# Kernel optimization log

Hardware: AMD Instinct MI355X
Metric: run time of the kernel (lower is better)

## Reference

```python
import jax, jax.numpy as jnp
import numpy as np

W, HN, C, NHEAD = 256, 128, 512, 8


def layer_norm(x, w, b, eps=1e-5):
    m = x.mean(-1, keepdims=True)
    v = ((x - m) ** 2).mean(-1, keepdims=True)
    return (x - m) / jnp.sqrt(v + eps) * w + b


def setup_inputs() -> dict:
    key = jax.random.key(0)
    ks = jax.random.split(key, 6)
    s = 0.02
    return {
        "feat_left": jax.random.normal(ks[0], (W, HN, C), jnp.float32),
        "feat_right": jax.random.normal(ks[1], (W, HN, C), jnp.float32),
        "pos": jax.random.normal(ks[2], (2 * W - 1, C), jnp.float32),
        "pos_indexes": jax.random.randint(ks[3], (W * W,), 0, 2 * W - 1, dtype=jnp.int32),
        "ln_w": jnp.ones((C,), jnp.float32),
        "ln_b": jnp.zeros((C,), jnp.float32),
        "in_proj_w": jax.random.normal(ks[4], (3 * C, C), jnp.float32) * s,
        "in_proj_b": jnp.zeros((3 * C,), jnp.float32),
        "out_w": jax.random.normal(ks[5], (C, C), jnp.float32) * s,
        "out_b": jnp.zeros((C,), jnp.float32),
    }


def reference(feat_left, feat_right, pos, pos_indexes, ln_w, ln_b, in_proj_w, in_proj_b, out_w, out_b):
    w, n, c = feat_left.shape
    e = NHEAD
    hd = c // e
    scaling = hd ** -0.5

    # pre-norm (same norm1 applied to both streams)
    ql = layer_norm(feat_left, ln_w, ln_b)     # [W,N,C]
    kv_in = layer_norm(feat_right, ln_w, ln_b)  # [W,N,C]

    # cross-attn projections: q from left with in_proj[:C], k/v from right with in_proj[C:]
    q = ql @ in_proj_w[:c].T + in_proj_b[:c]
    kv = kv_in @ in_proj_w[c:].T + in_proj_b[c:]
    k, v = jnp.split(kv, 2, axis=-1)

    # relative pos encoding gather: [2W-1,C] -> [W*W,C] -> [W,W',C]
    pe = pos[pos_indexes].reshape(w, w, c)
    qr_kr = pe @ in_proj_w[: 2 * c].T + in_proj_b[: 2 * c]
    q_r, k_r = jnp.split(qr_kr, 2, axis=-1)

    q = (q * scaling).reshape(w, n, e, hd)
    q_r = (q_r * scaling).reshape(w, w, e, hd)
    k = k.reshape(w, n, e, hd)
    v = v.reshape(w, n, e, hd)
    k_r = k_r.reshape(w, w, e, hd)

    # content-content + content-pos + pos-content scores: [N,E,W,W']
    attn = (jnp.einsum('wnec,vnec->newv', q, k)
            + jnp.einsum('wnec,wvec->newv', q, k_r)
            + jnp.einsum('vnec,wvec->newv', k, q_r))

    raw_attn = attn.sum(axis=1)                      # [N,W,W']
    p = jax.nn.softmax(attn, axis=-1)
    v_o = jnp.einsum('newv,vnec->wnec', p, v).reshape(w, n, c)
    v_o = v_o @ out_w.T + out_b

    return feat_left + v_o, raw_attn
```

## Files before the change

### kernel.cpp

```cpp
#include <hip/hip_runtime.h>

#define WW 256
#define NB 128
#define CD 512
#define NE 8
#define HD 64
#define NCHUNKS 4
#define SCALING 0.125f

typedef __attribute__((ext_vector_type(8))) short bfx8;
typedef __attribute__((ext_vector_type(4))) float fx4;

#define OFF_MEAN   0u
#define OFF_RSTD   65536u
#define OFF_WPB    131072u
#define OFF_OWB    524288u
#define OFF_S      655360u
#define OFF_U      656896u
#define OFF_PQ     658432u
#define OFF_PK     789504u
#define OFF_QB     920576u
#define OFF_KB     9309184u
#define OFF_VB     17697792u
#define OFF_ATTN   26086400u
#define OFF_T3     42863616u
#define OFF_PB     51252224u
#define OFF_VOB    59640832u

__device__ __forceinline__ unsigned short f2bf(float f) {
  unsigned u = __builtin_bit_cast(unsigned, f);
  u = (u + 0x7fffu + ((u >> 16) & 1u)) >> 16;
  return (unsigned short)u;
}
__device__ __forceinline__ float bf2f(unsigned short h) {
  unsigned u = ((unsigned)h) << 16;
  return __builtin_bit_cast(float, u);
}

#define GLDS16(g, l)                                                          \
  __builtin_amdgcn_global_load_lds(                                           \
      (const __attribute__((address_space(1))) void*)(g),                     \
      (__attribute__((address_space(3))) void*)(l), 16, 0, 0)

__global__ __launch_bounds__(256) void cvt_kernel(const float* __restrict__ a,
                                                  unsigned short* __restrict__ b,
                                                  int n8) {
  int i = blockIdx.x * 256 + threadIdx.x;
  if (i >= n8) return;
  float4 x = ((const float4*)a)[2 * i];
  float4 y = ((const float4*)a)[2 * i + 1];
  int4 o;
  o.x = (int)(((unsigned)f2bf(x.y) << 16) | f2bf(x.x));
  o.y = (int)(((unsigned)f2bf(x.w) << 16) | f2bf(x.z));
  o.z = (int)(((unsigned)f2bf(y.y) << 16) | f2bf(y.x));
  o.w = (int)(((unsigned)f2bf(y.w) << 16) | f2bf(y.z));
  ((int4*)b)[i] = o;
}

__global__ __launch_bounds__(256) void stats_kernel(const float* __restrict__ L,
                                                    const float* __restrict__ R,
                                                    float* __restrict__ mean,
                                                    float* __restrict__ rstd,
                                                    unsigned short* __restrict__ flb,
                                                    unsigned short* __restrict__ frb) {
  int wave = threadIdx.x >> 6, lane = threadIdx.x & 63;
  int row = blockIdx.x * 4 + wave;
  const float* src = (row < 32768) ? (L + (size_t)row * CD) : (R + (size_t)(row - 32768) * CD);
  unsigned short* drow = (row < 32768) ? (flb + (size_t)row * CD) : (frb + (size_t)(row - 32768) * CD);
  float4 a = *(const float4*)(src + lane * 4);
  float4 b = *(const float4*)(src + 256 + lane * 4);
  short4 sa, sb;
  sa.x = (short)f2bf(a.x); sa.y = (short)f2bf(a.y); sa.z = (short)f2bf(a.z); sa.w = (short)f2bf(a.w);
  sb.x = (short)f2bf(b.x); sb.y = (short)f2bf(b.y); sb.z = (short)f2bf(b.z); sb.w = (short)f2bf(b.w);
  *(short4*)(drow + lane * 4) = sa;
  *(short4*)(drow + 256 + lane * 4) = sb;
  float s  = a.x + a.y + a.z + a.w + b.x + b.y + b.z + b.w;
  float ss = a.x*a.x + a.y*a.y + a.z*a.z + a.w*a.w + b.x*b.x + b.y*b.y + b.z*b.z + b.w*b.w;
#pragma unroll
  for (int off = 32; off > 0; off >>= 1) {
    s  += __shfl_xor(s, off);
    ss += __shfl_xor(ss, off);
  }
  if (lane == 0) {
    float m = s * (1.0f / 512.0f);
    float v = ss * (1.0f / 512.0f) - m * m;
    mean[row] = m;
    rstd[row] = rsqrtf(v + 1e-5f);
  }
}

__global__ __launch_bounds__(256) void prep_kernel(const float* __restrict__ ipw,
                                                   const float* __restrict__ ipb,
                                                   const float* __restrict__ lnw,
                                                   const float* __restrict__ lnb,
                                                   unsigned short* __restrict__ Wpb,
                                                   float* __restrict__ S,
                                                   float* __restrict__ U) {
  int o = blockIdx.x, t = threadIdx.x;
  float s = 0.f, u = 0.f;
#pragma unroll
  for (int j0 = 0; j0 < 512; j0 += 256) {
    int j = j0 + t;
    float w0 = ipw[(size_t)o * 512 + j];
    float wl = w0 * lnw[j];
    unsigned short h = f2bf(wl);
    Wpb[(size_t)o * 512 + j] = h;
    s += bf2f(h);
    u += w0 * lnb[j];
  }
  __shared__ float rs[4], ru[4];
  int lane = t & 63, wv = t >> 6;
#pragma unroll
  for (int off = 32; off > 0; off >>= 1) { s += __shfl_xor(s, off); u += __shfl_xor(u, off); }
  if (lane == 0) { rs[wv] = s; ru[wv] = u; }
  __syncthreads();
  if (t == 0) {
    S[o] = rs[0] + rs[1] + rs[2] + rs[3];
    U[o] = ru[0] + ru[1] + ru[2] + ru[3] + ipb[o];
  }
}

__global__ __launch_bounds__(256) void gemm_ln(const unsigned short* __restrict__ A,
                                               const unsigned short* __restrict__ Bw,
                                               const float* __restrict__ S,
                                               const float* __restrict__ U,
                                               const float* __restrict__ mean,
                                               const float* __restrict__ rstd,
                                               unsigned short* __restrict__ out0,
                                               unsigned short* __restrict__ out1,
                                               int wOff, int statOff, float scale) {
  __shared__ unsigned short As[128 * 32];
  __shared__ unsigned short Bs[128 * 32];
  int t = threadIdx.x;
  int lane = t & 63, w = t >> 6;
  int quad = lane >> 4, l15 = lane & 15;
  int wm = w >> 1, wn = w & 1;
  int m0 = blockIdx.x * 128, n0 = blockIdx.y * 128;

  unsigned short* ldsA0 = As + (size_t)w * 16 * 32;
  unsigned short* ldsA1 = As + (size_t)(64 + w * 16) * 32;
  unsigned short* ldsB0 = Bs + (size_t)w * 16 * 32;
  unsigned short* ldsB1 = Bs + (size_t)(64 + w * 16) * 32;
  const unsigned short* gA0 = A + (size_t)(m0 + w * 16 + (lane >> 2)) * 512 + (lane & 3) * 8;
  const unsigned short* gA1 = gA0 + (size_t)64 * 512;
  const unsigned short* gB0 = Bw + (size_t)(wOff + n0 + w * 16 + (lane >> 2)) * 512 + (lane & 3) * 8;
  const unsigned short* gB1 = gB0 + (size_t)64 * 512;

  fx4 acc[4][4];
#pragma unroll
  for (int i = 0; i < 4; ++i)
#pragma unroll
    for (int j = 0; j < 4; ++j) acc[i][j] = (fx4){0.f, 0.f, 0.f, 0.f};

  for (int kt = 0; kt < 512; kt += 32) {
    GLDS16(gA0 + kt, ldsA0);
    GLDS16(gA1 + kt, ldsA1);
    GLDS16(gB0 + kt, ldsB0);
    GLDS16(gB1 + kt, ldsB1);
    __syncthreads();
    bfx8 af[4], bfr[4];
#pragma unroll
    for (int i = 0; i < 4; ++i)
      af[i] = *(const bfx8*)(As + (size_t)(wm * 64 + i * 16 + l15) * 32 + quad * 8);
#pragma unroll
    for (int j = 0; j < 4; ++j)
      bfr[j] = *(const bfx8*)(Bs + (size_t)(wn * 64 + j * 16 + l15) * 32 + quad * 8);
#pragma unroll
    for (int i = 0; i < 4; ++i)
#pragma unroll
      for (int j = 0; j < 4; ++j)
        acc[i][j] = __builtin_amdgcn_mfma_f32_16x16x32_bf16(af[i], bfr[j], acc[i][j], 0, 0, 0);
    __syncthreads();
  }

  float mn[16], rs[16];
#pragma unroll
  for (int i = 0; i < 4; ++i)
#pragma unroll
    for (int r = 0; r < 4; ++r) {
      int m = statOff + m0 + wm * 64 + i * 16 + quad * 4 + r;
      mn[i * 4 + r] = mean[m];
      rs[i * 4 + r] = rstd[m];
    }
#pragma unroll
  for (int j = 0; j < 4; ++j) {
    int oc = n0 + wn * 64 + j * 16 + l15;
    int o = wOff + oc;
    float Sv = S[o], Uv = U[o];
    unsigned short* dst; int cc;
    if (oc < 512) { dst = out0; cc = oc; } else { dst = out1; cc = oc - 512; }
#pragma unroll
    for (int i = 0; i < 4; ++i)
#pragma unroll
      for (int r = 0; r < 4; ++r) {
        int m = m0 + wm * 64 + i * 16 + quad * 4 + r;
        dst[(size_t)m * 512 + cc] =
            f2bf(((acc[i][j][r] - mn[i * 4 + r] * Sv) * rs[i * 4 + r] + Uv) * scale);
      }
  }
}

__global__ __launch_bounds__(256) void gemm_out(const unsigned short* __restrict__ A,
                                                const unsigned short* __restrict__ Bw,
                                                const float* __restrict__ ob,
                                                const float* __restrict__ fl,
                                                float* __restrict__ out, int wc) {
  __shared__ unsigned short As[128 * 32];
  __shared__ unsigned short Bs[128 * 32];
  int t = threadIdx.x;
  int lane = t & 63, w = t >> 6;
  int quad = lane >> 4, l15 = lane & 15;
  int wm = w >> 1, wn = w & 1;
  int n0 = blockIdx.x * 128, m0 = blockIdx.y * 128;

  unsigned short* ldsA0 = As + (size_t)w * 16 * 32;
  unsigned short* ldsA1 = As + (size_t)(64 + w * 16) * 32;
  unsigned short* ldsB0 = Bs + (size_t)w * 16 * 32;
  unsigned short* ldsB1 = Bs + (size_t)(64 + w * 16) * 32;
  const unsigned short* gA0 = A + (size_t)(m0 + w * 16 + (lane >> 2)) * 512 + (lane & 3) * 8;
  const unsigned short* gA1 = gA0 + (size_t)64 * 512;
  const unsigned short* gB0 = Bw + (size_t)(n0 + w * 16 + (lane >> 2)) * 512 + (lane & 3) * 8;
  const unsigned short* gB1 = gB0 + (size_t)64 * 512;

  fx4 acc[4][4];
#pragma unroll
  for (int i = 0; i < 4; ++i)
#pragma unroll
    for (int j = 0; j < 4; ++j) acc[i][j] = (fx4){0.f, 0.f, 0.f, 0.f};

  for (int kt = 0; kt < 512; kt += 32) {
    GLDS16(gA0 + kt, ldsA0);
    GLDS16(gA1 + kt, ldsA1);
    GLDS16(gB0 + kt, ldsB0);
    GLDS16(gB1 + kt, ldsB1);
    __syncthreads();
    bfx8 af[4], bfr[4];
#pragma unroll
    for (int i = 0; i < 4; ++i)
      af[i] = *(const bfx8*)(As + (size_t)(wm * 64 + i * 16 + l15) * 32 + quad * 8);
#pragma unroll
    for (int j = 0; j < 4; ++j)
      bfr[j] = *(const bfx8*)(Bs + (size_t)(wn * 64 + j * 16 + l15) * 32 + quad * 8);
#pragma unroll
    for (int i = 0; i < 4; ++i)
#pragma unroll
      for (int j = 0; j < 4; ++j)
        acc[i][j] = __builtin_amdgcn_mfma_f32_16x16x32_bf16(af[i], bfr[j], acc[i][j], 0, 0, 0);
    __syncthreads();
  }

  size_t gbase = (size_t)wc * 64 * NB * CD;
#pragma unroll
  for (int j = 0; j < 4; ++j) {
    int o = n0 + wn * 64 + j * 16 + l15;
    float bias = ob[o];
#pragma unroll
    for (int i = 0; i < 4; ++i)
#pragma unroll
      for (int r = 0; r < 4; ++r) {
        int m = m0 + wm * 64 + i * 16 + quad * 4 + r;
        size_t go = gbase + (size_t)m * 512 + o;
        out[go] = acc[i][j][r] + bias + fl[go];
      }
  }
}

__device__ __forceinline__ void compute16(const float* __restrict__ As,
                                          const float* __restrict__ Bs,
                                          float acc[4][4], int tx, int ty) {
#pragma unroll
  for (int kk = 0; kk < 16; ++kk) {
    float4 av = *(const float4*)(As + kk * 64 + ty * 4);
    float4 bv = *(const float4*)(Bs + kk * 64 + tx * 4);
    const float aa[4] = {av.x, av.y, av.z, av.w};
    const float bb[4] = {bv.x, bv.y, bv.z, bv.w};
#pragma unroll
    for (int i = 0; i < 4; ++i)
#pragma unroll
      for (int j = 0; j < 4; ++j)
        acc[i][j] = fmaf(aa[i], bb[j], acc[i][j]);
  }
}

__global__ __launch_bounds__(256) void posproj_kernel(const float* __restrict__ pos,
                                                      const float* __restrict__ ipw,
                                                      const float* __restrict__ ipb,
                                                      unsigned short* __restrict__ Pq,
                                                      unsigned short* __restrict__ Pk) {
  __shared__ float As[16 * 64], Bs[16 * 64];
  int t = threadIdx.x, tx = t & 15, ty = t >> 4;
  int n0 = blockIdx.x * 64, m0 = blockIdx.y * 64;
  int lr = t >> 2, lq = t & 3;
  int arow = m0 + lr; if (arow > 510) arow = 510;
  const float* xrow = pos + (size_t)arow * 512 + lq * 4;
  const float* wrow = ipw + (size_t)(n0 + lr) * 512 + lq * 4;
  float acc[4][4] = {};
  for (int kt = 0; kt < 512; kt += 16) {
    float4 a = *(const float4*)(xrow + kt);
    float4 b = *(const float4*)(wrow + kt);
    __syncthreads();
    As[(lq * 4 + 0) * 64 + lr] = a.x; As[(lq * 4 + 1) * 64 + lr] = a.y;
    As[(lq * 4 + 2) * 64 + lr] = a.z; As[(lq * 4 + 3) * 64 + lr] = a.w;
    Bs[(lq * 4 + 0) * 64 + lr] = b.x; Bs[(lq * 4 + 1) * 64 + lr] = b.y;
    Bs[(lq * 4 + 2) * 64 + lr] = b.z; Bs[(lq * 4 + 3) * 64 + lr] = b.w;
    __syncthreads();
    compute16(As, Bs, acc, tx, ty);
  }
  float scale = (n0 < 512) ? SCALING : 1.0f;
  unsigned short* dst; int co;
  if (n0 < 512) { dst = Pq; co = n0; } else { dst = Pk; co = n0 - 512; }
#pragma unroll
  for (int i = 0; i < 4; ++i) {
    int m = m0 + ty * 4 + i;
    if (m < 511) {
      short4 r;
      r.x = (short)f2bf((acc[i][0] + ipb[n0 + tx * 4 + 0]) * scale);
      r.y = (short)f2bf((acc[i][1] + ipb[n0 + tx * 4 + 1]) * scale);
      r.z = (short)f2bf((acc[i][2] + ipb[n0 + tx * 4 + 2]) * scale);
      r.w = (short)f2bf((acc[i][3] + ipb[n0 + tx * 4 + 3]) * scale);
      *(short4*)(dst + (size_t)m * 512 + co + tx * 4) = r;
    }
  }
}

__global__ __launch_bounds__(256) void t3_kernel(const unsigned short* __restrict__ kb,
                                                 const unsigned short* __restrict__ Pq,
                                                 const int* __restrict__ idx,
                                                 unsigned short* __restrict__ T3, int wc) {
  __shared__ unsigned short As[128 * 72];
  __shared__ unsigned short Bs[64 * 72];
  int t = threadIdx.x, lane = t & 63, w = t >> 6;
  int quad = lane >> 4, l15 = lane & 15;
  int e = blockIdx.x, v = blockIdx.y;
  const unsigned short* asrc = kb + ((size_t)v * NB) * 512 + e * 64;
  for (int c = t; c < 1024; c += 256) {
    int row = c >> 3, c8 = c & 7;
    *(int4*)(As + row * 72 + c8 * 8) = *(const int4*)(asrc + (size_t)row * 512 + c8 * 8);
  }
  for (int c = t; c < 512; c += 256) {
    int row = c >> 3, c8 = c & 7;
    int ri = idx[(wc * 64 + row) * WW + v];
    *(int4*)(Bs + row * 72 + c8 * 8) = *(const int4*)(Pq + (size_t)ri * 512 + e * 64 + c8 * 8);
  }
  __syncthreads();
  fx4 acc[2][4];
#pragma unroll
  for (int i = 0; i < 2; ++i)
#pragma unroll
    for (int j = 0; j < 4; ++j) acc[i][j] = (fx4){0.f, 0.f, 0.f, 0.f};
#pragma unroll
  for (int kt = 0; kt < 64; kt += 32) {
    bfx8 af[2], bfr[4];
#pragma unroll
    for (int i = 0; i < 2; ++i)
      af[i] = *(const bfx8*)(As + (w * 32 + i * 16 + l15) * 72 + kt + quad * 8);
#pragma unroll
    for (int j = 0; j < 4; ++j)
      bfr[j] = *(const bfx8*)(Bs + (j * 16 + l15) * 72 + kt + quad * 8);
#pragma unroll
    for (int i = 0; i < 2; ++i)
#pragma unroll
      for (int j = 0; j < 4; ++j)
        acc[i][j] = __builtin_amdgcn_mfma_f32_16x16x32_bf16(af[i], bfr[j], acc[i][j], 0, 0, 0);
  }
#pragma unroll
  for (int i = 0; i < 2; ++i)
#pragma unroll
    for (int j = 0; j < 4; ++j)
#pragma unroll
      for (int r = 0; r < 4; ++r) {
        int n = w * 32 + i * 16 + quad * 4 + r;
        int wq = j * 16 + l15;
        T3[(((size_t)e * WW + v) * NB + n) * 64 + wq] = f2bf(acc[i][j][r]);
      }
}

__global__ __launch_bounds__(256) void t1_kernel(const unsigned short* __restrict__ qb,
                                                 const unsigned short* __restrict__ kb,
                                                 const unsigned short* __restrict__ T3,
                                                 float* __restrict__ attn, int wc) {
  __shared__ unsigned short As[64 * 72];
  __shared__ unsigned short Bs[256 * 72];
  int t = threadIdx.x, lane = t & 63, w = t >> 6;
  int quad = lane >> 4, l15 = lane & 15;
  int e = blockIdx.x, n = blockIdx.y;
  const unsigned short* asrc = qb + ((size_t)(wc * 64) * NB + n) * 512 + e * 64;
  for (int c = t; c < 512; c += 256) {
    int row = c >> 3, c8 = c & 7;
    *(int4*)(As + row * 72 + c8 * 8) = *(const int4*)(asrc + (size_t)row * NB * 512 + c8 * 8);
  }
  const unsigned short* bsrc = kb + (size_t)n * 512 + e * 64;
  for (int c = t; c < 2048; c += 256) {
    int row = c >> 3, c8 = c & 7;
    *(int4*)(Bs + row * 72 + c8 * 8) = *(const int4*)(bsrc + (size_t)row * NB * 512 + c8 * 8);
  }
  __syncthreads();
  fx4 acc[4][4];
#pragma unroll
  for (int i = 0; i < 4; ++i)
#pragma unroll
    for (int j = 0; j < 4; ++j) acc[i][j] = (fx4){0.f, 0.f, 0.f, 0.f};
#pragma unroll
  for (int kt = 0; kt < 64; kt += 32) {
    bfx8 af[4], bfr[4];
#pragma unroll
    for (int i = 0; i < 4; ++i)
      af[i] = *(const bfx8*)(As + (i * 16 + l15) * 72 + kt + quad * 8);
#pragma unroll
    for (int j = 0; j < 4; ++j)
      bfr[j] = *(const bfx8*)(Bs + (w * 64 + j * 16 + l15) * 72 + kt + quad * 8);
#pragma unroll
    for (int i = 0; i < 4; ++i)
#pragma unroll
      for (int j = 0; j < 4; ++j)
        acc[i][j] = __builtin_amdgcn_mfma_f32_16x16x32_bf16(af[i], bfr[j], acc[i][j], 0, 0, 0);
  }
  __syncthreads();
  const unsigned short* tsrc = T3 + ((size_t)e * WW * NB + n) * 64;
  for (int c = t; c < 2048; c += 256) {
    int row = c >> 3, c8 = c & 7;
    *(int4*)(Bs + row * 72 + c8 * 8) = *(const int4*)(tsrc + (size_t)row * NB * 64 + c8 * 8);
  }
  __syncthreads();
#pragma unroll
  for (int i = 0; i < 4; ++i)
#pragma unroll
    for (int j = 0; j < 4; ++j) {
      int vg = w * 64 + j * 16 + l15;
      ushort4 t3v = *(const ushort4*)(Bs + (size_t)vg * 72 + i * 16 + quad * 4);
      const unsigned short tv[4] = {t3v.x, t3v.y, t3v.z, t3v.w};
#pragma unroll
      for (int r = 0; r < 4; ++r) {
        int wq = i * 16 + quad * 4 + r;
        float* p = attn + (((size_t)n * NE + e) * 64 + wq) * WW + vg;
        *p = acc[i][j][r] + bf2f(tv[r]);
      }
    }
}

__global__ __launch_bounds__(256) void t2s_kernel(const unsigned short* __restrict__ qb,
                                                  const unsigned short* __restrict__ Pk,
                                                  const int* __restrict__ idx,
                                                  const float* __restrict__ attn,
                                                  unsigned short* __restrict__ pbuf,
                                                  float* __restrict__ raw, int wc) {
  __shared__ unsigned short As[16 * 72];
  __shared__ unsigned short Bs[256 * 72];
  __shared__ int idxs[256];
  __shared__ float redm[16 * 4];
  __shared__ float reds[16 * 4];
  int t = threadIdx.x, lane = t & 63, w = t >> 6;
  int quad = lane >> 4, l15 = lane & 15;
  int wq = blockIdx.x, nt = blockIdx.y;
  int n0 = nt * 16;
  idxs[t] = idx[((size_t)(wc * 64 + wq)) * WW + t];

  fx4 raws[4];
#pragma unroll
  for (int j = 0; j < 4; ++j) raws[j] = (fx4){0.f, 0.f, 0.f, 0.f};

  const unsigned short* abase = qb + ((size_t)(wc * 64 + wq) * NB + n0) * 512;

  for (int e = 0; e < NE; ++e) {
    __syncthreads();
    if (t < 128) {
      int row = t >> 3, c8 = t & 7;
      *(int4*)(As + row * 72 + c8 * 8) = *(const int4*)(abase + (size_t)row * 512 + e * 64 + c8 * 8);
    }
    for (int c = t; c < 2048; c += 256) {
      int row = c >> 3, c8 = c & 7;
      int ri = idxs[row];
      *(int4*)(Bs + row * 72 + c8 * 8) = *(const int4*)(Pk + (size_t)ri * 512 + e * 64 + c8 * 8);
    }
    __syncthreads();

    fx4 acc[4];
#pragma unroll
    for (int j = 0; j < 4; ++j) acc[j] = (fx4){0.f, 0.f, 0.f, 0.f};
    bfx8 af0 = *(const bfx8*)(As + l15 * 72 + quad * 8);
    bfx8 af1 = *(const bfx8*)(As + l15 * 72 + 32 + quad * 8);
#pragma unroll
    for (int j = 0; j < 4; ++j) {
      bfx8 b0 = *(const bfx8*)(Bs + (w * 64 + j * 16 + l15) * 72 + quad * 8);
      acc[j] = __builtin_amdgcn_mfma_f32_16x16x32_bf16(af0, b0, acc[j], 0, 0, 0);
    }
#pragma unroll
    for (int j = 0; j < 4; ++j) {
      bfx8 b1 = *(const bfx8*)(Bs + (w * 64 + j * 16 + l15) * 72 + 32 + quad * 8);
      acc[j] = __builtin_amdgcn_mfma_f32_16x16x32_bf16(af1, b1, acc[j], 0, 0, 0);
    }

#pragma unroll
    for (int j = 0; j < 4; ++j) {
      int vg = w * 64 + j * 16 + l15;
#pragma unroll
      for (int r = 0; r < 4; ++r) {
        int n = n0 + quad * 4 + r;
        acc[j][r] += attn[(((size_t)n * NE + e) * 64 + wq) * WW + vg];
      }
    }

    float rm[4];
#pragma unroll
    for (int r = 0; r < 4; ++r)
      rm[r] = fmaxf(fmaxf(acc[0][r], acc[1][r]), fmaxf(acc[2][r], acc[3][r]));
#pragma unroll
    for (int off = 1; off < 16; off <<= 1)
#pragma unroll
      for (int r = 0; r < 4; ++r) rm[r] = fmaxf(rm[r], __shfl_xor(rm[r], off));
    if (l15 == 0) {
#pragma unroll
      for (int r = 0; r < 4; ++r) redm[(quad * 4 + r) * 4 + w] = rm[r];
    }
    __syncthreads();
    float fm[4];
#pragma unroll
    for (int r = 0; r < 4; ++r) {
      const float* rp = redm + (quad * 4 + r) * 4;
      fm[r] = fmaxf(fmaxf(rp[0], rp[1]), fmaxf(rp[2], rp[3]));
    }
    float ex[4][4];
    float ls[4] = {0.f, 0.f, 0.f, 0.f};
#pragma unroll
    for (int j = 0; j < 4; ++j)
#pragma unroll
      for (int r = 0; r < 4; ++r) {
        ex[j][r] = __expf(acc[j][r] - fm[r]);
        ls[r] += ex[j][r];
      }
#pragma unroll
    for (int off = 1; off < 16; off <<= 1)
#pragma unroll
      for (int r = 0; r < 4; ++r) ls[r] += __shfl_xor(ls[r], off);
    if (l15 == 0) {
#pragma unroll
      for (int r = 0; r < 4; ++r) reds[(quad * 4 + r) * 4 + w] = ls[r];
    }
    __syncthreads();
    float inv[4];
#pragma unroll
    for (int r = 0; r < 4; ++r) {
      const float* sp = reds + (quad * 4 + r) * 4;
      inv[r] = 1.0f / (sp[0] + sp[1] + sp[2] + sp[3]);
    }
#pragma unroll
    for (int j = 0; j < 4; ++j) {
      int vg = w * 64 + j * 16 + l15;
#pragma unroll
      for (int r = 0; r < 4; ++r) {
        int n = n0 + quad * 4 + r;
        pbuf[(((size_t)n * NE + e) * 64 + wq) * WW + vg] = f2bf(ex[j][r] * inv[r]);
        raws[j][r] += acc[j][r];
      }
    }
  }

#pragma unroll
  for (int j = 0; j < 4; ++j) {
    int vg = w * 64 + j * 16 + l15;
#pragma unroll
    for (int r = 0; r < 4; ++r) {
      int n = n0 + quad * 4 + r;
      raw[((size_t)n * WW + wc * 64 + wq) * WW + vg] = raws[j][r];
    }
  }
}

__global__ __launch_bounds__(256) void pv_kernel(const unsigned short* __restrict__ pb,
                                                 const unsigned short* __restrict__ vb,
                                                 unsigned short* __restrict__ vob) {
  __shared__ unsigned short As[64 * 72];
  __shared__ unsigned short Bs[64 * 72];
  int t = threadIdx.x, lane = t & 63, w = t >> 6;
  int quad = lane >> 4, l15 = lane & 15;
  int e = blockIdx.x, n = blockIdx.y;
  fx4 acc[4];
#pragma unroll
  for (int j = 0; j < 4; ++j) acc[j] = (fx4){0.f, 0.f, 0.f, 0.f};
  const unsigned short* abase = pb + (((size_t)n * NE + e) * 64) * WW;
  for (int kc = 0; kc < 4; ++kc) {
    for (int c = t; c < 512; c += 256) {
      int row = c >> 3, c8 = c & 7;
      *(int4*)(As + row * 72 + c8 * 8) = *(const int4*)(abase + (size_t)row * WW + kc * 64 + c8 * 8);
    }
    for (int c = t; c < 512; c += 256) {
      int row = c >> 3, c8 = c & 7;
      *(int4*)(Bs + row * 72 + c8 * 8) =
          *(const int4*)(vb + ((size_t)(kc * 64 + row) * NB + n) * 512 + e * 64 + c8 * 8);
    }
    __syncthreads();
#pragma unroll
    for (int kt = 0; kt < 64; kt += 32) {
      bfx8 af = *(const bfx8*)(As + (w * 16 + l15) * 72 + kt + quad * 8);
      bfx8 bfr[4];
#pragma unroll
      for (int j = 0; j < 4; ++j)
        bfr[j] = *(const bfx8*)(Bs + (j * 16 + l15) * 72 + kt + quad * 8);
#pragma unroll
      for (int j = 0; j < 4; ++j)
        acc[j] = __builtin_amdgcn_mfma_f32_16x16x32_bf16(af, bfr[j], acc[j], 0, 0, 0);
    }
    __syncthreads();
  }
#pragma unroll
  for (int j = 0; j < 4; ++j)
#pragma unroll
    for (int r = 0; r < 4; ++r) {
      int wq = w * 16 + quad * 4 + r;
      vob[((size_t)wq * NB + n) * 512 + e * 64 + j * 16 + l15] = f2bf(acc[j][r]);
    }
}

extern "C" void kernel_launch(void* const* d_in, const int* in_sizes, int n_in,
                              void* d_out, int out_size, void* d_ws, size_t ws_size,
                              hipStream_t stream) {
  const float* fl  = (const float*)d_in[0];
  const float* fr  = (const float*)d_in[1];
  const float* pos = (const float*)d_in[2];
  const int*  pidx = (const int*)d_in[3];
  const float* lnw = (const float*)d_in[4];
  const float* lnb = (const float*)d_in[5];
  const float* ipw = (const float*)d_in[6];
  const float* ipb = (const float*)d_in[7];
  const float* ow  = (const float*)d_in[8];
  const float* ob  = (const float*)d_in[9];

  float* ws   = (float*)d_ws;
  float* mean = ws + OFF_MEAN;
  float* rstd = ws + OFF_RSTD;
  unsigned short* Wpb = (unsigned short*)(ws + OFF_WPB);
  unsigned short* owb = (unsigned short*)(ws + OFF_OWB);
  float* S    = ws + OFF_S;
  float* U    = ws + OFF_U;
  unsigned short* Pq = (unsigned short*)(ws + OFF_PQ);
  unsigned short* Pk = (unsigned short*)(ws + OFF_PK);
  unsigned short* qb = (unsigned short*)(ws + OFF_QB);
  unsigned short* kb = (unsigned short*)(ws + OFF_KB);
  unsigned short* vb = (unsigned short*)(ws + OFF_VB);
  float* attn = ws + OFF_ATTN;
  unsigned short* T3  = (unsigned short*)(ws + OFF_T3);
  unsigned short* pb  = (unsigned short*)(ws + OFF_PB);
  unsigned short* vob = (unsigned short*)(ws + OFF_VOB);
  unsigned short* flb = (unsigned short*)(ws + OFF_ATTN);
  unsigned short* frb = flb + (size_t)32768 * 512;

  float* outF = (float*)d_out;
  float* outR = outF + (size_t)WW * NB * CD;

  stats_kernel<<<16384, 256, 0, stream>>>(fl, fr, mean, rstd, flb, frb);
  prep_kernel<<<1536, 256, 0, stream>>>(ipw, ipb, lnw, lnb, Wpb, S, U);
  cvt_kernel<<<128, 256, 0, stream>>>(ow, owb, 32768);
  posproj_kernel<<<dim3(16, 8), 256, 0, stream>>>(pos, ipw, ipb, Pq, Pk);
  gemm_ln<<<dim3(256, 4), 256, 0, stream>>>(flb, Wpb, S, U, mean, rstd, qb, qb, 0, 0, SCALING);
  gemm_ln<<<dim3(256, 8), 256, 0, stream>>>(frb, Wpb, S, U, mean, rstd, kb, vb, 512, 32768, 1.0f);

  for (int wc = 0; wc < NCHUNKS; ++wc) {
    t3_kernel<<<dim3(8, 256), 256, 0, stream>>>(kb, Pq, pidx, T3, wc);
    t1_kernel<<<dim3(8, 128), 256, 0, stream>>>(qb, kb, T3, attn, wc);
    t2s_kernel<<<dim3(64, 8), 256, 0, stream>>>(qb, Pk, pidx, attn, pb, outR, wc);
    pv_kernel<<<dim3(8, 128), 256, 0, stream>>>(pb, vb, vob);
    gemm_out<<<dim3(4, 64), 256, 0, stream>>>(vob, owb, ob, fl, outF, wc);
  }
}
```

Measured before the change: 841.6 us.

## Double-buffer GEMM LDS tiles with XOR swizzle and move pos projection to MFMA

The gemm_ln and gemm_out kernels now double-buffer their LDS tiles, so the global-to-LDS load of the next K slice is issued before computing the current one. They also XOR-swizzle the LDS column layout to reduce bank conflicts. The fp32 FMA position-projection kernel is replaced by a bf16 MFMA GEMM, which needs extra conversion kernels for pos and in_proj_w. This doubles LDS use per block and adds custom waitcnt and barrier sequencing, which must be exactly right to avoid races.

```diff
diff --git a/kernel.cpp b/kernel.cpp
--- a/kernel.cpp
+++ b/kernel.cpp
@@ -129,21 +129,20 @@
                                                unsigned short* __restrict__ out0,
                                                unsigned short* __restrict__ out1,
                                                int wOff, int statOff, float scale) {
-  __shared__ unsigned short As[128 * 32];
-  __shared__ unsigned short Bs[128 * 32];
+  __shared__ unsigned short As[2][128 * 32];
+  __shared__ unsigned short Bs[2][128 * 32];
   int t = threadIdx.x;
   int lane = t & 63, w = t >> 6;
   int quad = lane >> 4, l15 = lane & 15;
   int wm = w >> 1, wn = w & 1;
   int m0 = blockIdx.x * 128, n0 = blockIdx.y * 128;
 
-  unsigned short* ldsA0 = As + (size_t)w * 16 * 32;
-  unsigned short* ldsA1 = As + (size_t)(64 + w * 16) * 32;
-  unsigned short* ldsB0 = Bs + (size_t)w * 16 * 32;
-  unsigned short* ldsB1 = Bs + (size_t)(64 + w * 16) * 32;
-  const unsigned short* gA0 = A + (size_t)(m0 + w * 16 + (lane >> 2)) * 512 + (lane & 3) * 8;
+  int cs = ((lane & 3) ^ ((lane >> 3) & 3)) * 8;
+  unsigned lo0 = (unsigned)(w * 16) * 32;
+  unsigned lo1 = (unsigned)(64 + w * 16) * 32;
+  const unsigned short* gA0 = A + (size_t)(m0 + w * 16 + (lane >> 2)) * 512 + cs;
   const unsigned short* gA1 = gA0 + (size_t)64 * 512;
-  const unsigned short* gB0 = Bw + (size_t)(wOff + n0 + w * 16 + (lane >> 2)) * 512 + (lane & 3) * 8;
+  const unsigned short* gB0 = Bw + (size_t)(wOff + n0 + w * 16 + (lane >> 2)) * 512 + cs;
   const unsigned short* gB1 = gB0 + (size_t)64 * 512;
 
   fx4 acc[4][4];
@@ -152,26 +151,51 @@
 #pragma unroll
     for (int j = 0; j < 4; ++j) acc[i][j] = (fx4){0.f, 0.f, 0.f, 0.f};
 
-  for (int kt = 0; kt < 512; kt += 32) {
-    GLDS16(gA0 + kt, ldsA0);
-    GLDS16(gA1 + kt, ldsA1);
-    GLDS16(gB0 + kt, ldsB0);
-    GLDS16(gB1 + kt, ldsB1);
-    __syncthreads();
-    bfx8 af[4], bfr[4];
-#pragma unroll
-    for (int i = 0; i < 4; ++i)
-      af[i] = *(const bfx8*)(As + (size_t)(wm * 64 + i * 16 + l15) * 32 + quad * 8);
-#pragma unroll
-    for (int j = 0; j < 4; ++j)
-      bfr[j] = *(const bfx8*)(Bs + (size_t)(wn * 64 + j * 16 + l15) * 32 + quad * 8);
-#pragma unroll
-    for (int i = 0; i < 4; ++i)
-#pragma unroll
-      for (int j = 0; j < 4; ++j)
-        acc[i][j] = __builtin_amdgcn_mfma_f32_16x16x32_bf16(af[i], bfr[j], acc[i][j], 0, 0, 0);
-    __syncthreads();
-  }
+  int ro = (quad ^ ((l15 >> 1) & 3)) * 8;
+
+#define STAGE_G(buf, kk)                                                      \
+  do {                                                                        \
+    GLDS16(gA0 + (kk), &As[buf][lo0]);                                        \
+    GLDS16(gA1 + (kk), &As[buf][lo1]);                                        \
+    GLDS16(gB0 + (kk), &Bs[buf][lo0]);                                        \
+    GLDS16(gB1 + (kk), &Bs[buf][lo1]);                                        \
+  } while (0)
+
+#define COMPUTE_G(buf)                                                        \
+  do {                                                                        \
+    const unsigned short* Ab = &As[buf][0];                                   \
+    const unsigned short* Bb = &Bs[buf][0];                                   \
+    bfx8 af[4], bfr[4];                                                       \
+    _Pragma("unroll")                                                         \
+    for (int i = 0; i < 4; ++i)                                               \
+      af[i] = *(const bfx8*)(Ab + (size_t)(wm * 64 + i * 16 + l15) * 32 + ro);\
+    _Pragma("unroll")                                                         \
+    for (int j = 0; j < 4; ++j)                                               \
+      bfr[j] = *(const bfx8*)(Bb + (size_t)(wn * 64 + j * 16 + l15) * 32 + ro);\
+    _Pragma("unroll")                                                         \
+    for (int i = 0; i < 4; ++i)                                               \
+      _Pragma("unroll")                                                       \
+      for (int j = 0; j < 4; ++j)                                             \
+        acc[i][j] = __builtin_amdgcn_mfma_f32_16x16x32_bf16(af[i], bfr[j], acc[i][j], 0, 0, 0); \
+  } while (0)
+
+  STAGE_G(0, 0);
+  int cur = 0;
+  for (int kt = 0; kt < 480; kt += 32) {
+    STAGE_G(cur ^ 1, kt + 32);
+    asm volatile("s_waitcnt vmcnt(4)" ::: "memory");
+    __builtin_amdgcn_s_barrier();
+    __builtin_amdgcn_sched_barrier(0);
+    COMPUTE_G(cur);
+    asm volatile("s_waitcnt lgkmcnt(0)" ::: "memory");
+    __builtin_amdgcn_s_barrier();
+    __builtin_amdgcn_sched_barrier(0);
+    cur ^= 1;
+  }
+  asm volatile("s_waitcnt vmcnt(0)" ::: "memory");
+  __builtin_amdgcn_s_barrier();
+  __builtin_amdgcn_sched_barrier(0);
+  COMPUTE_G(cur);
 
   float mn[16], rs[16];
 #pragma unroll
@@ -198,6 +222,8 @@
             f2bf(((acc[i][j][r] - mn[i * 4 + r] * Sv) * rs[i * 4 + r] + Uv) * scale);
       }
   }
+#undef STAGE_G
+#undef COMPUTE_G
 }
 
 __global__ __launch_bounds__(256) void gemm_out(const unsigned short* __restrict__ A,
@@ -205,21 +231,20 @@
                                                 const float* __restrict__ ob,
                                                 const float* __restrict__ fl,
                                                 float* __restrict__ out, int wc) {
-  __shared__ unsigned short As[128 * 32];
-  __shared__ unsigned short Bs[128 * 32];
+  __shared__ unsigned short As[2][128 * 32];
+  __shared__ unsigned short Bs[2][128 * 32];
   int t = threadIdx.x;
   int lane = t & 63, w = t >> 6;
   int quad = lane >> 4, l15 = lane & 15;
   int wm = w >> 1, wn = w & 1;
   int n0 = blockIdx.x * 128, m0 = blockIdx.y * 128;
 
-  unsigned short* ldsA0 = As + (size_t)w * 16 * 32;
-  unsigned short* ldsA1 = As + (size_t)(64 + w * 16) * 32;
-  unsigned short* ldsB0 = Bs + (size_t)w * 16 * 32;
-  unsigned short* ldsB1 = Bs + (size_t)(64 + w * 16) * 32;
-  const unsigned short* gA0 = A + (size_t)(m0 + w * 16 + (lane >> 2)) * 512 + (lane & 3) * 8;
+  int cs = ((lane & 3) ^ ((lane >> 3) & 3)) * 8;
+  unsigned lo0 = (unsigned)(w * 16) * 32;
+  unsigned lo1 = (unsigned)(64 + w * 16) * 32;
+  const unsigned short* gA0 = A + (size_t)(m0 + w * 16 + (lane >> 2)) * 512 + cs;
   const unsigned short* gA1 = gA0 + (size_t)64 * 512;
-  const unsigned short* gB0 = Bw + (size_t)(n0 + w * 16 + (lane >> 2)) * 512 + (lane & 3) * 8;
+  const unsigned short* gB0 = Bw + (size_t)(n0 + w * 16 + (lane >> 2)) * 512 + cs;
   const unsigned short* gB1 = gB0 + (size_t)64 * 512;
 
   fx4 acc[4][4];
@@ -228,26 +253,51 @@
 #pragma unroll
     for (int j = 0; j < 4; ++j) acc[i][j] = (fx4){0.f, 0.f, 0.f, 0.f};
 
-  for (int kt = 0; kt < 512; kt += 32) {
-    GLDS16(gA0 + kt, ldsA0);
-    GLDS16(gA1 + kt, ldsA1);
-    GLDS16(gB0 + kt, ldsB0);
-    GLDS16(gB1 + kt, ldsB1);
-    __syncthreads();
-    bfx8 af[4], bfr[4];
-#pragma unroll
-    for (int i = 0; i < 4; ++i)
-      af[i] = *(const bfx8*)(As + (size_t)(wm * 64 + i * 16 + l15) * 32 + quad * 8);
-#pragma unroll
-    for (int j = 0; j < 4; ++j)
-      bfr[j] = *(const bfx8*)(Bs + (size_t)(wn * 64 + j * 16 + l15) * 32 + quad * 8);
-#pragma unroll
-    for (int i = 0; i < 4; ++i)
-#pragma unroll
-      for (int j = 0; j < 4; ++j)
-        acc[i][j] = __builtin_amdgcn_mfma_f32_16x16x32_bf16(af[i], bfr[j], acc[i][j], 0, 0, 0);
-    __syncthreads();
-  }
+  int ro = (quad ^ ((l15 >> 1) & 3)) * 8;
+
+#define STAGE_O(buf, kk)                                                      \
+  do {                                                                        \
+    GLDS16(gA0 + (kk), &As[buf][lo0]);                                        \
+    GLDS16(gA1 + (kk), &As[buf][lo1]);                                        \
+    GLDS16(gB0 + (kk), &Bs[buf][lo0]);                                        \
+    GLDS16(gB1 + (kk), &Bs[buf][lo1]);                                        \
+  } while (0)
+
+#define COMPUTE_O(buf)                                                        \
+  do {                                                                        \
+    const unsigned short* Ab = &As[buf][0];                                   \
+    const unsigned short* Bb = &Bs[buf][0];                                   \
+    bfx8 af[4], bfr[4];                                                       \
+    _Pragma("unroll")                                                         \
+    for (int i = 0; i < 4; ++i)                                               \
+      af[i] = *(const bfx8*)(Ab + (size_t)(wm * 64 + i * 16 + l15) * 32 + ro);\
+    _Pragma("unroll")                                                         \
+    for (int j = 0; j < 4; ++j)                                               \
+      bfr[j] = *(const bfx8*)(Bb + (size_t)(wn * 64 + j * 16 + l15) * 32 + ro);\
+    _Pragma("unroll")                                                         \
+    for (int i = 0; i < 4; ++i)                                               \
+      _Pragma("unroll")                                                       \
+      for (int j = 0; j < 4; ++j)                                             \
+        acc[i][j] = __builtin_amdgcn_mfma_f32_16x16x32_bf16(af[i], bfr[j], acc[i][j], 0, 0, 0); \
+  } while (0)
+
+  STAGE_O(0, 0);
+  int cur = 0;
+  for (int kt = 0; kt < 480; kt += 32) {
+    STAGE_O(cur ^ 1, kt + 32);
+    asm volatile("s_waitcnt vmcnt(4)" ::: "memory");
+    __builtin_amdgcn_s_barrier();
+    __builtin_amdgcn_sched_barrier(0);
+    COMPUTE_O(cur);
+    asm volatile("s_waitcnt lgkmcnt(0)" ::: "memory");
+    __builtin_amdgcn_s_barrier();
+    __builtin_amdgcn_sched_barrier(0);
+    cur ^= 1;
+  }
+  asm volatile("s_waitcnt vmcnt(0)" ::: "memory");
+  __builtin_amdgcn_s_barrier();
+  __builtin_amdgcn_sched_barrier(0);
+  COMPUTE_O(cur);
 
   size_t gbase = (size_t)wc * 64 * NB * CD;
 #pragma unroll
@@ -263,64 +313,103 @@
         out[go] = acc[i][j][r] + bias + fl[go];
       }
   }
-}
-
-__device__ __forceinline__ void compute16(const float* __restrict__ As,
-                                          const float* __restrict__ Bs,
-                                          float acc[4][4], int tx, int ty) {
-#pragma unroll
-  for (int kk = 0; kk < 16; ++kk) {
-    float4 av = *(const float4*)(As + kk * 64 + ty * 4);
-    float4 bv = *(const float4*)(Bs + kk * 64 + tx * 4);
-    const float aa[4] = {av.x, av.y, av.z, av.w};
-    const float bb[4] = {bv.x, bv.y, bv.z, bv.w};
+#undef STAGE_O
+#undef COMPUTE_O
+}
+
+__global__ __launch_bounds__(256) void posproj_mfma(const unsigned short* __restrict__ Apos,
+                                                    const unsigned short* __restrict__ Bw,
+                                                    const float* __restrict__ ipb,
+                                                    unsigned short* __restrict__ Pq,
+                                                    unsigned short* __restrict__ Pk) {
+  __shared__ unsigned short As[2][128 * 32];
+  __shared__ unsigned short Bs[2][128 * 32];
+  int t = threadIdx.x;
+  int lane = t & 63, w = t >> 6;
+  int quad = lane >> 4, l15 = lane & 15;
+  int wm = w >> 1, wn = w & 1;
+  int m0 = blockIdx.x * 128, n0 = blockIdx.y * 128;
+
+  int cs = ((lane & 3) ^ ((lane >> 3) & 3)) * 8;
+  unsigned lo0 = (unsigned)(w * 16) * 32;
+  unsigned lo1 = (unsigned)(64 + w * 16) * 32;
+  int ar0 = m0 + w * 16 + (lane >> 2); if (ar0 > 510) ar0 = 510;
+  int ar1 = m0 + 64 + w * 16 + (lane >> 2); if (ar1 > 510) ar1 = 510;
+  const unsigned short* gA0 = Apos + (size_t)ar0 * 512 + cs;
+  const unsigned short* gA1 = Apos + (size_t)ar1 * 512 + cs;
+  const unsigned short* gB0 = Bw + (size_t)(n0 + w * 16 + (lane >> 2)) * 512 + cs;
+  const unsigned short* gB1 = gB0 + (size_t)64 * 512;
+
+  fx4 acc[4][4];
+#pragma unroll
+  for (int i = 0; i < 4; ++i)
+#pragma unroll
+    for (int j = 0; j < 4; ++j) acc[i][j] = (fx4){0.f, 0.f, 0.f, 0.f};
+
+  int ro = (quad ^ ((l15 >> 1) & 3)) * 8;
+
+#define STAGE_P(buf, kk)                                                      \
+  do {                                                                        \
+    GLDS16(gA0 + (kk), &As[buf][lo0]);                                        \
+    GLDS16(gA1 + (kk), &As[buf][lo1]);                                        \
+    GLDS16(gB0 + (kk), &Bs[buf][lo0]);                                        \
+    GLDS16(gB1 + (kk), &Bs[buf][lo1]);                                        \
+  } while (0)
+
+#define COMPUTE_P(buf)                                                        \
+  do {                                                                        \
+    const unsigned short* Ab = &As[buf][0];                                   \
+    const unsigned short* Bb = &Bs[buf][0];                                   \
+    bfx8 af[4], bfr[4];                                                       \
+    _Pragma("unroll")                                                         \
+    for (int i = 0; i < 4; ++i)                                               \
+      af[i] = *(const bfx8*)(Ab + (size_t)(wm * 64 + i * 16 + l15) * 32 + ro);\
+    _Pragma("unroll")                                                         \
+    for (int j = 0; j < 4; ++j)                                               \
+      bfr[j] = *(const bfx8*)(Bb + (size_t)(wn * 64 + j * 16 + l15) * 32 + ro);\
+    _Pragma("unroll")                                                         \
+    for (int i = 0; i < 4; ++i)                                               \
+      _Pragma("unroll")                                                       \
+      for (int j = 0; j < 4; ++j)                                             \
+        acc[i][j] = __builtin_amdgcn_mfma_f32_16x16x32_bf16(af[i], bfr[j], acc[i][j], 0, 0, 0); \
+  } while (0)
+
+  STAGE_P(0, 0);
+  int cur = 0;
+  for (int kt = 0; kt < 480; kt += 32) {
+    STAGE_P(cur ^ 1, kt + 32);
+    asm volatile("s_waitcnt vmcnt(4)" ::: "memory");
+    __builtin_amdgcn_s_barrier();
+    __builtin_amdgcn_sched_barrier(0);
+    COMPUTE_P(cur);
+    asm volatile("s_waitcnt lgkmcnt(0)" ::: "memory");
+    __builtin_amdgcn_s_barrier();
+    __builtin_amdgcn_sched_barrier(0);
+    cur ^= 1;
+  }
+  asm volatile("s_waitcnt vmcnt(0)" ::: "memory");
+  __builtin_amdgcn_s_barrier();
+  __builtin_amdgcn_sched_barrier(0);
+  COMPUTE_P(cur);
+
+#pragma unroll
+  for (int j = 0; j < 4; ++j) {
+    int o = n0 + wn * 64 + j * 16 + l15;
+    float bias = ipb[o];
+    float scale = (o < 512) ? SCALING : 1.0f;
+    unsigned short* dst; int cc;
+    if (o < 512) { dst = Pq; cc = o; } else { dst = Pk; cc = o - 512; }
 #pragma unroll
     for (int i = 0; i < 4; ++i)
 #pragma unroll
-      for (int j = 0; j < 4; ++j)
-        acc[i][j] = fmaf(aa[i], bb[j], acc[i][j]);
-  }
-}
-
-__global__ __launch_bounds__(256) void posproj_kernel(const float* __restrict__ pos,
-                                                      const float* __restrict__ ipw,
-                                                      const float* __restrict__ ipb,
-                                                      unsigned short* __restrict__ Pq,
-                                                      unsigned short* __restrict__ Pk) {
-  __shared__ float As[16 * 64], Bs[16 * 64];
-  int t = threadIdx.x, tx = t & 15, ty = t >> 4;
-  int n0 = blockIdx.x * 64, m0 = blockIdx.y * 64;
-  int lr = t >> 2, lq = t & 3;
-  int arow = m0 + lr; if (arow > 510) arow = 510;
-  const float* xrow = pos + (size_t)arow * 512 + lq * 4;
-  const float* wrow = ipw + (size_t)(n0 + lr) * 512 + lq * 4;
-  float acc[4][4] = {};
-  for (int kt = 0; kt < 512; kt += 16) {
-    float4 a = *(const float4*)(xrow + kt);
-    float4 b = *(const float4*)(wrow + kt);
-    __syncthreads();
-    As[(lq * 4 + 0) * 64 + lr] = a.x; As[(lq * 4 + 1) * 64 + lr] = a.y;
-    As[(lq * 4 + 2) * 64 + lr] = a.z; As[(lq * 4 + 3) * 64 + lr] = a.w;
-    Bs[(lq * 4 + 0) * 64 + lr] = b.x; Bs[(lq * 4 + 1) * 64 + lr] = b.y;
-    Bs[(lq * 4 + 2) * 64 + lr] = b.z; Bs[(lq * 4 + 3) * 64 + lr] = b.w;
-    __syncthreads();
-    compute16(As, Bs, acc, tx, ty);
-  }
-  float scale = (n0 < 512) ? SCALING : 1.0f;
-  unsigned short* dst; int co;
-  if (n0 < 512) { dst = Pq; co = n0; } else { dst = Pk; co = n0 - 512; }
-#pragma unroll
-  for (int i = 0; i < 4; ++i) {
-    int m = m0 + ty * 4 + i;
-    if (m < 511) {
-      short4 r;
-      r.x = (short)f2bf((acc[i][0] + ipb[n0 + tx * 4 + 0]) * scale);
-      r.y = (short)f2bf((acc[i][1] + ipb[n0 + tx * 4 + 1]) * scale);
-      r.z = (short)f2bf((acc[i][2] + ipb[n0 + tx * 4 + 2]) * scale);
-      r.w = (short)f2bf((acc[i][3] + ipb[n0 + tx * 4 + 3]) * scale);
-      *(short4*)(dst + (size_t)m * 512 + co + tx * 4) = r;
-    }
-  }
+      for (int r = 0; r < 4; ++r) {
+        int m = m0 + wm * 64 + i * 16 + quad * 4 + r;
+        if (m < 511)
+          dst[(size_t)m * 512 + cc] = f2bf((acc[i][j][r] + bias) * scale);
+      }
+  }
+#undef STAGE_P
+#undef COMPUTE_P
 }
 
 __global__ __launch_bounds__(256) void t3_kernel(const unsigned short* __restrict__ kb,
@@ -643,6 +732,8 @@
   unsigned short* vob = (unsigned short*)(ws + OFF_VOB);
   unsigned short* flb = (unsigned short*)(ws + OFF_ATTN);
   unsigned short* frb = flb + (size_t)32768 * 512;
+  unsigned short* posb = (unsigned short*)(ws + OFF_T3);
+  unsigned short* ipwb = posb + 262144;
 
   float* outF = (float*)d_out;
   float* outR = outF + (size_t)WW * NB * CD;
@@ -650,7 +741,9 @@
   stats_kernel<<<16384, 256, 0, stream>>>(fl, fr, mean, rstd, flb, frb);
   prep_kernel<<<1536, 256, 0, stream>>>(ipw, ipb, lnw, lnb, Wpb, S, U);
   cvt_kernel<<<128, 256, 0, stream>>>(ow, owb, 32768);
-  posproj_kernel<<<dim3(16, 8), 256, 0, stream>>>(pos, ipw, ipb, Pq, Pk);
+  cvt_kernel<<<128, 256, 0, stream>>>(pos, posb, 32704);
+  cvt_kernel<<<256, 256, 0, stream>>>(ipw, ipwb, 65536);
+  posproj_mfma<<<dim3(4, 8), 256, 0, stream>>>(posb, ipwb, ipb, Pq, Pk);
   gemm_ln<<<dim3(256, 4), 256, 0, stream>>>(flb, Wpb, S, U, mean, rstd, qb, qb, 0, 0, SCALING);
   gemm_ln<<<dim3(256, 8), 256, 0, stream>>>(frb, Wpb, S, U, mean, rstd, kb, vb, 512, 32768, 1.0f);
 
```

After: 825.0 us. -2.0%, faster.
